# Kernel optimization log

Hardware: AMD Instinct MI355X
Metric: run time of the kernel (lower is better)

The kernel has to match this reference:

```python
import jax, jax.numpy as jnp
import numpy as np

HIDDEN = 1024
NUM_HEADS = 16
HEAD_DIM = HIDDEN // NUM_HEADS
ROPE_BASE = 10000.0
LN_EPS = 1e-8


def _rope_cos_sin(seq_len, dim, dtype=jnp.float32):
    inv_freq = 1.0 / (ROPE_BASE ** (jnp.arange(0, dim, 2, dtype=jnp.float32) / dim))
    t = jnp.arange(seq_len, dtype=jnp.float32)
    freqs = jnp.einsum('i,j->ij', t, inv_freq)          # [S, dim/2]
    emb = jnp.concatenate([freqs, freqs], axis=-1)       # [S, dim]
    return jnp.cos(emb).astype(dtype), jnp.sin(emb).astype(dtype)


def _rotate_half(x):
    x1, x2 = jnp.split(x, 2, axis=-1)
    return jnp.concatenate([-x2, x1], axis=-1)


def setup_inputs() -> dict:
    key = jax.random.key(0)
    ks = jax.random.split(key, 8)
    B, S, H = 4, 2048, HIDDEN
    x = jax.random.normal(ks[0], (B, S, H), dtype=jnp.float32)
    # causal mask, True = attend
    attn_mask = jnp.tril(jnp.ones((S, S), dtype=bool))[None].repeat(B, axis=0)
    lim_p = 1.0 / np.sqrt(H)
    Wp = jax.random.uniform(ks[1], (H, 4 * H), minval=-lim_p, maxval=lim_p, dtype=jnp.float32)
    bp = jax.random.uniform(ks[2], (4 * H,), minval=-lim_p, maxval=lim_p, dtype=jnp.float32)
    ln_g = jnp.ones((H,), dtype=jnp.float32)
    ln_b = jnp.zeros((H,), dtype=jnp.float32)
    Wt = jax.random.uniform(ks[3], (H, H), minval=-lim_p, maxval=lim_p, dtype=jnp.float32)
    bt = jax.random.uniform(ks[4], (H,), minval=-lim_p, maxval=lim_p, dtype=jnp.float32)
    return {"x": x, "attn_mask": attn_mask, "Wp": Wp, "bp": bp,
            "ln_g": ln_g, "ln_b": ln_b, "Wt": Wt, "bt": bt}


def reference(x, attn_mask, Wp, bp, ln_g, ln_b, Wt, bt):
    B, S, H = x.shape
    nh, hd = NUM_HEADS, HEAD_DIM
    proj = x @ Wp + bp                                   # [B,S,4H]
    U, V, Q, K = jnp.split(proj, 4, axis=-1)
    # [B, nh, S, hd]
    Q = Q.reshape(B, S, nh, hd).transpose(0, 2, 1, 3)
    K = K.reshape(B, S, nh, hd).transpose(0, 2, 1, 3)
    V = V.reshape(B, S, nh, hd).transpose(0, 2, 1, 3)
    cos, sin = _rope_cos_sin(S, hd, x.dtype)             # [S, hd]
    Qr = Q * cos + _rotate_half(Q) * sin
    Kr = K * cos + _rotate_half(K) * sin
    scale = hd ** -0.5
    scores = jnp.einsum('bhqd,bhkd->bhqk', Qr, Kr) * scale
    # masked positions -> sigmoid(-inf) == 0; use where for grad safety
    attn = jnp.where(attn_mask[:, None, :, :], jax.nn.sigmoid(scores), 0.0)
    attn_out = jnp.einsum('bhqk,bhkd->bhqd', attn, V)
    attn_out = attn_out.transpose(0, 2, 1, 3).reshape(B, S, H)
    mu = jnp.mean(attn_out, axis=-1, keepdims=True)
    var = jnp.var(attn_out, axis=-1, keepdims=True)
    attn_out = (attn_out - mu) / jnp.sqrt(var + LN_EPS) * ln_g + ln_b
    gated = jax.nn.silu(U) * attn_out
    out = gated @ Wt + bt
    return x + out
```

## Files before the change

### kernel.cpp

```cpp
#include <hip/hip_runtime.h>
#include <math.h>

#define H 1024
#define NH 16
#define HD 64
#define B_ 4
#define S_ 2048
#define ROWS (B_*S_)

#define QSCALE (-0.1803368801111664f)
#define ROPE_C (9.210340371976184f / 32.0f)

typedef __bf16 bf16x2_t __attribute__((ext_vector_type(2)));
typedef __bf16 bf16x4_t __attribute__((ext_vector_type(4)));
typedef __bf16 bf16x8_t __attribute__((ext_vector_type(8)));
typedef float floatx4_t __attribute__((ext_vector_type(4)));

#define GLOAD_LDS16(gp, lp)                                                        \
    __builtin_amdgcn_global_load_lds(                                              \
        (const __attribute__((address_space(1))) unsigned int*)(gp),               \
        (__attribute__((address_space(3))) unsigned int*)(lp), 16, 0, 0)

__global__ __launch_bounds__(256)
void convert_x(const float* __restrict__ src, __bf16* __restrict__ dst)
{
    int i = blockIdx.x * blockDim.x + threadIdx.x;
    float4 v = *reinterpret_cast<const float4*>(&src[(size_t)i * 4]);
    bf16x4_t w = { (__bf16)v.x, (__bf16)v.y, (__bf16)v.z, (__bf16)v.w };
    *reinterpret_cast<bf16x4_t*>(&dst[(size_t)i * 4]) = w;
}

__global__ __launch_bounds__(256)
void transpose_cvt(const float* __restrict__ W, __bf16* __restrict__ Wt, int K, int N)
{
    __shared__ __bf16 t[32][33];
    const int tx = threadIdx.x & 31, ty = threadIdx.x >> 5;
    const int bn = blockIdx.x * 32, bk = blockIdx.y * 32;
#pragma unroll
    for (int i = 0; i < 4; i++) {
        int r = ty + i * 8;
        t[tx][r] = (__bf16)W[(size_t)(bk + r) * N + bn + tx];
    }
    __syncthreads();
#pragma unroll
    for (int i = 0; i < 4; i++) {
        int r = ty + i * 8;
        Wt[(size_t)(bn + r) * K + bk + tx] = t[r][tx];
    }
}


__global__ __launch_bounds__(256)
void gemm_out(const __bf16* __restrict__ A, const __bf16* __restrict__ Bt,
              const float* __restrict__ bias, const float* __restrict__ resid,
              float* __restrict__ C, int M, int N, int K)
{
    __shared__ __bf16 As[128 * 32];
    __shared__ __bf16 Bs[128 * 32];

    const int tid  = threadIdx.x;
    const int wave = tid >> 6, lane = tid & 63;
    const int quad = lane >> 4, ln = lane & 15;
    const int wm = wave & 1, wn = wave >> 1;
    const int m0 = blockIdx.y * 128, n0 = blockIdx.x * 128;

    const int srow = lane >> 2;
    const int skc  = (((lane & 3) ^ ((srow >> 1) & 3)) * 8);
    const int qsw  = (quad ^ ((ln >> 1) & 3)) * 8;

    floatx4_t acc[4][4];
#pragma unroll
    for (int i = 0; i < 4; i++)
#pragma unroll
        for (int j = 0; j < 4; j++) acc[i][j] = (floatx4_t){0.f, 0.f, 0.f, 0.f};

    for (int k0 = 0; k0 < K; k0 += 32) {
#pragma unroll
        for (int p = 0; p < 2; p++) {
            int i = wave * 2 + p;
            int rl = i * 16 + srow;
            GLOAD_LDS16(A  + (size_t)(m0 + rl) * K + k0 + skc, &As[i * 512]);
            GLOAD_LDS16(Bt + (size_t)(n0 + rl) * K + k0 + skc, &Bs[i * 512]);
        }
        __syncthreads();

        bf16x8_t af[4], bf[4];
#pragma unroll
        for (int mt = 0; mt < 4; mt++)
            af[mt] = *reinterpret_cast<const bf16x8_t*>(&As[(wm * 64 + mt * 16 + ln) * 32 + qsw]);
#pragma unroll
        for (int nt = 0; nt < 4; nt++)
            bf[nt] = *reinterpret_cast<const bf16x8_t*>(&Bs[(wn * 64 + nt * 16 + ln) * 32 + qsw]);
#pragma unroll
        for (int mt = 0; mt < 4; mt++)
#pragma unroll
            for (int nt = 0; nt < 4; nt++)
                acc[mt][nt] = __builtin_amdgcn_mfma_f32_16x16x32_bf16(af[mt], bf[nt], acc[mt][nt], 0, 0, 0);
        __syncthreads();
    }

#pragma unroll
    for (int mt = 0; mt < 4; mt++) {
#pragma unroll
        for (int nt = 0; nt < 4; nt++) {
            int col = n0 + wn * 64 + nt * 16 + ln;
            float bv = bias[col];
#pragma unroll
            for (int reg = 0; reg < 4; reg++) {
                int row = m0 + wm * 64 + mt * 16 + quad * 4 + reg;
                float v = acc[mt][nt][reg] + bv + resid[(size_t)row * N + col];
                C[(size_t)row * N + col] = v;
            }
        }
    }
}

__global__ __launch_bounds__(256)
void gemm_proj(const __bf16* __restrict__ A, const __bf16* __restrict__ Bt,
               const float* __restrict__ bias,
               __bf16* __restrict__ Ug, __bf16* __restrict__ Vh,
               __bf16* __restrict__ Qh, __bf16* __restrict__ Kh)
{
    const int M = ROWS, N = 4096, K = 1024;
    __shared__ __bf16 As[128 * 32];
    __shared__ __bf16 Bs[128 * 32];

    const int tid  = threadIdx.x;
    const int wave = tid >> 6, lane = tid & 63;
    const int quad = lane >> 4, ln = lane & 15;
    const int wm = wave & 1, wn = wave >> 1;
    const int m0 = blockIdx.y * 128, n0 = blockIdx.x * 128;

    const int srow = lane >> 2;
    const int skc  = (((lane & 3) ^ ((srow >> 1) & 3)) * 8);
    const int qsw  = (quad ^ ((ln >> 1) & 3)) * 8;

    floatx4_t acc[4][4];
#pragma unroll
    for (int i = 0; i < 4; i++)
#pragma unroll
        for (int j = 0; j < 4; j++) acc[i][j] = (floatx4_t){0.f, 0.f, 0.f, 0.f};

    for (int k0 = 0; k0 < K; k0 += 32) {
#pragma unroll
        for (int p = 0; p < 2; p++) {
            int i = wave * 2 + p;
            int rl = i * 16 + srow;
            GLOAD_LDS16(A  + (size_t)(m0 + rl) * K + k0 + skc, &As[i * 512]);
            GLOAD_LDS16(Bt + (size_t)(n0 + rl) * K + k0 + skc, &Bs[i * 512]);
        }
        __syncthreads();

        bf16x8_t af[4], bf[4];
#pragma unroll
        for (int mt = 0; mt < 4; mt++)
            af[mt] = *reinterpret_cast<const bf16x8_t*>(&As[(wm * 64 + mt * 16 + ln) * 32 + qsw]);
#pragma unroll
        for (int nt = 0; nt < 4; nt++)
            bf[nt] = *reinterpret_cast<const bf16x8_t*>(&Bs[(wn * 64 + nt * 16 + ln) * 32 + qsw]);
#pragma unroll
        for (int mt = 0; mt < 4; mt++)
#pragma unroll
            for (int nt = 0; nt < 4; nt++)
                acc[mt][nt] = __builtin_amdgcn_mfma_f32_16x16x32_bf16(af[mt], bf[nt], acc[mt][nt], 0, 0, 0);
        __syncthreads();
    }

    float bv[4];
#pragma unroll
    for (int nt = 0; nt < 4; nt++) bv[nt] = bias[n0 + wn * 64 + nt * 16 + ln];

    if (n0 < 1024) {
#pragma unroll
        for (int mt = 0; mt < 4; mt++)
#pragma unroll
            for (int nt = 0; nt < 4; nt++) {
                int col = n0 + wn * 64 + nt * 16 + ln;
#pragma unroll
                for (int reg = 0; reg < 4; reg++) {
                    int row = m0 + wm * 64 + mt * 16 + quad * 4 + reg;
                    Ug[(size_t)row * 1024 + col] = (__bf16)(acc[mt][nt][reg] + bv[nt]);
                }
            }
    } else if (n0 < 2048) {
        const int h = ((n0 - 1024) >> 6) + wn;
#pragma unroll
        for (int mt = 0; mt < 4; mt++)
#pragma unroll
            for (int reg = 0; reg < 4; reg++) {
                int row = m0 + wm * 64 + mt * 16 + quad * 4 + reg;
                int b = row >> 11, s = row & (S_ - 1);
                size_t orow = ((size_t)(b * NH + h) * S_ + s) * 64;
#pragma unroll
                for (int nt = 0; nt < 4; nt++)
                    Vh[orow + nt * 16 + ln] = (__bf16)(acc[mt][nt][reg] + bv[nt]);
            }
    } else {
        const bool isQ = (n0 < 3072);
        const int h = ((n0 - (isQ ? 2048 : 3072)) >> 6) + wn;
        __bf16* dst = isQ ? Qh : Kh;
        const float sc = isQ ? QSCALE : 1.0f;
        const float inv0 = __expf(-(float)ln * ROPE_C);
        const float inv1 = __expf(-(float)(16 + ln) * ROPE_C);
#pragma unroll
        for (int mt = 0; mt < 4; mt++)
#pragma unroll
            for (int reg = 0; reg < 4; reg++) {
                int row = m0 + wm * 64 + mt * 16 + quad * 4 + reg;
                int b = row >> 11, s = row & (S_ - 1);
                size_t orow = ((size_t)(b * NH + h) * S_ + s) * 64;
                float sn0, cs0, sn1, cs1;
                __sincosf((float)s * inv0, &sn0, &cs0);
                __sincosf((float)s * inv1, &sn1, &cs1);
                float lo0 = acc[0][0][reg], hi0 = acc[0][2][reg];
                float lo1 = acc[0][1][reg], hi1 = acc[0][3][reg];
                lo0 = acc[mt][0][reg] + bv[0]; hi0 = acc[mt][2][reg] + bv[2];
                lo1 = acc[mt][1][reg] + bv[1]; hi1 = acc[mt][3][reg] + bv[3];
                dst[orow + ln]      = (__bf16)((lo0 * cs0 - hi0 * sn0) * sc);
                dst[orow + 32 + ln] = (__bf16)((hi0 * cs0 + lo0 * sn0) * sc);
                dst[orow + 16 + ln] = (__bf16)((lo1 * cs1 - hi1 * sn1) * sc);
                dst[orow + 48 + ln] = (__bf16)((hi1 * cs1 + lo1 * sn1) * sc);
            }
    }
}

__global__ __launch_bounds__(256)
void transpose_v(const __bf16* __restrict__ Vh, __bf16* __restrict__ VtG)
{
    const int tid = threadIdx.x;
    const int st = blockIdx.x, bh = blockIdx.y;
    const int s0 = st * 64;
    const int d = tid & 63, k16 = tid >> 6;
    __bf16 vals[16];
#pragma unroll
    for (int j = 0; j < 16; j++) {
        int k = s0 + k16 * 16 + j;
        vals[j] = Vh[((size_t)bh * S_ + k) * 64 + d];
    }
    size_t orow = ((size_t)(bh * 64 + d)) * S_ + s0 + k16 * 16;
    *reinterpret_cast<bf16x8_t*>(&VtG[orow])     = *reinterpret_cast<bf16x8_t*>(&vals[0]);
    *reinterpret_cast<bf16x8_t*>(&VtG[orow + 8]) = *reinterpret_cast<bf16x8_t*>(&vals[8]);
}

__global__ __launch_bounds__(256)
void attn_mfma(const __bf16* __restrict__ Qh, const __bf16* __restrict__ Kh,
               const __bf16* __restrict__ VtG, __bf16* __restrict__ attn_out)
{
    __shared__ __bf16 Ks[4096];
    __shared__ __bf16 Vt[4096];
    __shared__ __bf16 Ps[4][32][72];

    const int tid = threadIdx.x, wave = tid >> 6, lane = tid & 63;
    const int quad = lane >> 4, ln = lane & 15;
    const int qt = (S_ / 128 - 1) - (blockIdx.x >> 6);
    const int hb = blockIdx.x & 63, h = hb & 15, b = hb >> 4, bh = b * NH + h;
    const int Q0 = qt * 128, T0 = 2 * qt;
    const int wl = wave * 16 + ln;

    const size_t qr = ((size_t)bh * S_ + Q0 + wl) * 64;
    bf16x8_t qa[2][2];
    qa[0][0] = *reinterpret_cast<const bf16x8_t*>(&Qh[qr + quad * 8]);
    qa[0][1] = *reinterpret_cast<const bf16x8_t*>(&Qh[qr + 32 + quad * 8]);
    qa[1][0] = *reinterpret_cast<const bf16x8_t*>(&Qh[qr + 4096 + quad * 8]);
    qa[1][1] = *reinterpret_cast<const bf16x8_t*>(&Qh[qr + 4096 + 32 + quad * 8]);

    const int sr = lane >> 3, scl = (lane & 7) ^ sr;
    const int c0 = wave * 2, c1 = c0 + 1;
    const size_t khead = (size_t)bh * S_ * 64;
    const int koff0 = (c0 * 8 + sr) * 64 + scl * 8;
    const int koff1 = (c1 * 8 + sr) * 64 + scl * 8;
    const size_t vg0 = ((size_t)bh * 64 + c0 * 8 + sr) * S_ + scl * 8;
    const size_t vg1 = ((size_t)bh * 64 + c1 * 8 + sr) * S_ + scl * 8;

    const int m7 = ln & 7;
    int ka[4][2];
#pragma unroll
    for (int nt = 0; nt < 4; nt++) {
        int row = nt * 16 + ln;
        ka[nt][0] = row * 64 + ((quad ^ m7) << 3);
        ka[nt][1] = row * 64 + (((quad + 4) ^ m7) << 3);
    }

    floatx4_t o[2][4];
#pragma unroll
    for (int s = 0; s < 2; s++)
#pragma unroll
        for (int dt = 0; dt < 4; dt++) o[s][dt] = (floatx4_t){0.f, 0.f, 0.f, 0.f};

    for (int kt = 0; kt <= T0 + 1; kt++) {
        __syncthreads();
        const size_t kg = khead + (size_t)kt * 4096;
        GLOAD_LDS16(Kh  + kg + koff0, &Ks[c0 * 512]);
        GLOAD_LDS16(Kh  + kg + koff1, &Ks[c1 * 512]);
        GLOAD_LDS16(VtG + vg0 + kt * 64, &Vt[c0 * 512]);
        GLOAD_LDS16(VtG + vg1 + kt * 64, &Vt[c1 * 512]);
        __syncthreads();

        bf16x8_t kf[4][2];
#pragma unroll
        for (int nt = 0; nt < 4; nt++) {
            kf[nt][0] = *reinterpret_cast<const bf16x8_t*>(&Ks[ka[nt][0]]);
            kf[nt][1] = *reinterpret_cast<const bf16x8_t*>(&Ks[ka[nt][1]]);
        }
        bf16x8_t vf[4][2];
#pragma unroll
        for (int dt = 0; dt < 4; dt++) {
            vf[dt][0] = *reinterpret_cast<const bf16x8_t*>(&Vt[ka[dt][0]]);
            vf[dt][1] = *reinterpret_cast<const bf16x8_t*>(&Vt[ka[dt][1]]);
        }

        const int mode0 = (kt < T0) ? 0 : ((kt == T0) ? 1 : 2);
        const int mode1 = (kt <= T0) ? 0 : 1;

#pragma unroll
        for (int s = 0; s < 2; s++) {
            const int mode = s ? mode1 : mode0;
            if (mode == 2) continue;

            floatx4_t st[4];
#pragma unroll
            for (int nt = 0; nt < 4; nt++) {
                floatx4_t acc = (floatx4_t){0.f, 0.f, 0.f, 0.f};
                acc = __builtin_amdgcn_mfma_f32_16x16x32_bf16(kf[nt][0], qa[s][0], acc, 0, 0, 0);
                acc = __builtin_amdgcn_mfma_f32_16x16x32_bf16(kf[nt][1], qa[s][1], acc, 0, 0, 0);
                st[nt] = acc;
            }

#pragma unroll
            for (int nt = 0; nt < 4; nt++) {
                bf16x4_t pk;
#pragma unroll
                for (int r = 0; r < 4; r++) {
                    float a = st[nt][r];
                    if (mode == 1) {
                        int kl = nt * 16 + quad * 4 + r;
                        a = (kl <= wl) ? a : __builtin_inff();
                    }
                    float p = __builtin_amdgcn_rcpf(1.f + __builtin_amdgcn_exp2f(a));
                    pk[r] = (__bf16)p;
                }
                *reinterpret_cast<bf16x4_t*>(&Ps[wave][s * 16 + ln][nt * 16 + quad * 4]) = pk;
            }

            const __bf16* prow = &Ps[wave][s * 16 + ln][quad * 8];
            bf16x8_t p0 = *reinterpret_cast<const bf16x8_t*>(prow);
            bf16x8_t p1 = *reinterpret_cast<const bf16x8_t*>(prow + 32);
#pragma unroll
            for (int dt = 0; dt < 4; dt++) {
                o[s][dt] = __builtin_amdgcn_mfma_f32_16x16x32_bf16(p0, vf[dt][0], o[s][dt], 0, 0, 0);
                o[s][dt] = __builtin_amdgcn_mfma_f32_16x16x32_bf16(p1, vf[dt][1], o[s][dt], 0, 0, 0);
            }
        }
    }

#pragma unroll
    for (int s = 0; s < 2; s++) {
        const int qrow_g = b * S_ + Q0 + s * 64 + wave * 16 + quad * 4;
#pragma unroll
        for (int dt = 0; dt < 4; dt++) {
#pragma unroll
            for (int reg = 0; reg < 4; reg++) {
                attn_out[(size_t)(qrow_g + reg) * H + h * 64 + dt * 16 + ln] =
                    (__bf16)o[s][dt][reg];
            }
        }
    }
}

__global__ __launch_bounds__(256)
void ln_gate_kernel(const __bf16* __restrict__ attn_out, const __bf16* __restrict__ Ug,
                    const float* __restrict__ ln_g, const float* __restrict__ ln_b,
                    __bf16* __restrict__ gated)
{
    const int row = blockIdx.x;
    const int tid = threadIdx.x;

    bf16x4_t vb = *reinterpret_cast<const bf16x4_t*>(&attn_out[(size_t)row * H + tid * 4]);
    float v0 = (float)vb[0], v1 = (float)vb[1], v2 = (float)vb[2], v3 = (float)vb[3];
    float s  = v0 + v1 + v2 + v3;
    float sq = v0 * v0 + v1 * v1 + v2 * v2 + v3 * v3;
#pragma unroll
    for (int off = 32; off > 0; off >>= 1) {
        s  += __shfl_down(s, off);
        sq += __shfl_down(sq, off);
    }
    __shared__ float ps[4], pq[4];
    int wave = tid >> 6, lane = tid & 63;
    if (lane == 0) { ps[wave] = s; pq[wave] = sq; }
    __syncthreads();
    float ts = ps[0] + ps[1] + ps[2] + ps[3];
    float tq = pq[0] + pq[1] + pq[2] + pq[3];
    float mu  = ts * (1.f / (float)H);
    float var = tq * (1.f / (float)H) - mu * mu;
    float rstd = rsqrtf(var + 1e-8f);

    bf16x4_t ub = *reinterpret_cast<const bf16x4_t*>(&Ug[(size_t)row * 1024 + tid * 4]);
    float4 g  = *reinterpret_cast<const float4*>(&ln_g[tid * 4]);
    float4 bb = *reinterpret_cast<const float4*>(&ln_b[tid * 4]);
    float u0 = (float)ub[0], u1 = (float)ub[1], u2 = (float)ub[2], u3 = (float)ub[3];
    bf16x4_t outv;
    outv[0] = (__bf16)(((v0 - mu) * rstd * g.x + bb.x) * (u0 / (1.f + __expf(-u0))));
    outv[1] = (__bf16)(((v1 - mu) * rstd * g.y + bb.y) * (u1 / (1.f + __expf(-u1))));
    outv[2] = (__bf16)(((v2 - mu) * rstd * g.z + bb.z) * (u2 / (1.f + __expf(-u2))));
    outv[3] = (__bf16)(((v3 - mu) * rstd * g.w + bb.w) * (u3 / (1.f + __expf(-u3))));
    *reinterpret_cast<bf16x4_t*>(&gated[(size_t)row * H + tid * 4]) = outv;
}

extern "C" void kernel_launch(void* const* d_in, const int* in_sizes, int n_in,
                              void* d_out, int out_size, void* d_ws, size_t ws_size,
                              hipStream_t stream)
{
    const float* x    = (const float*)d_in[0];
    const float* Wp   = (const float*)d_in[2];
    const float* bp   = (const float*)d_in[3];
    const float* ln_g = (const float*)d_in[4];
    const float* ln_b = (const float*)d_in[5];
    const float* Wt   = (const float*)d_in[6];
    const float* bt   = (const float*)d_in[7];
    float* out = (float*)d_out;

    char* ws = (char*)d_ws;
    const size_t MB = 1024 * 1024;
    __bf16* Ug    = (__bf16*)(ws);
    __bf16* Vh    = (__bf16*)(ws + 16  * MB);
    __bf16* Qh    = (__bf16*)(ws + 32  * MB);
    __bf16* Kh    = (__bf16*)(ws + 48  * MB);
    __bf16* attn  = (__bf16*)(ws + 64  * MB);
    __bf16* gated = (__bf16*)(ws + 80  * MB);
    __bf16* VtG   = (__bf16*)(ws + 96  * MB);
    __bf16* Ax    = (__bf16*)(ws + 112 * MB);
    __bf16* Wp_t  = (__bf16*)(ws + 128 * MB);
    __bf16* Wt_t  = (__bf16*)(ws + 136 * MB);

    convert_x<<<(ROWS * H / 4) / 256, 256, 0, stream>>>(x, Ax);
    transpose_cvt<<<dim3(4096 / 32, 1024 / 32), 256, 0, stream>>>(Wp, Wp_t, 1024, 4096);
    transpose_cvt<<<dim3(1024 / 32, 1024 / 32), 256, 0, stream>>>(Wt, Wt_t, 1024, 1024);

    dim3 g1(4096 / 128, ROWS / 128);
    gemm_proj<<<g1, 256, 0, stream>>>(Ax, Wp_t, bp, Ug, Vh, Qh, Kh);

    transpose_v<<<dim3(S_ / 64, B_ * NH), 256, 0, stream>>>(Vh, VtG);

    attn_mfma<<<(S_ / 128) * NH * B_, 256, 0, stream>>>(Qh, Kh, VtG, attn);

    ln_gate_kernel<<<ROWS, 256, 0, stream>>>(attn, Ug, ln_g, ln_b, gated);

    dim3 g3(1024 / 128, ROWS / 128);
    gemm_out<<<g3, 256, 0, stream>>>(gated, Wt_t, bt, x, out, ROWS, 1024, 1024);
}
```

Before: 345.2 us.

## Double-buffer LDS tiles in GEMMs and attention, merge prep kernels into one launch

Both GEMM kernels and the attention kernel now use two LDS buffers. The next K tile is fetched with global_load_lds while MFMAs run on the current tile, which removes one barrier per iteration. The three preprocessing kernels (x conversion and two weight transposes) are merged into one launch dispatched by block index, and the per-wave P scratch in attention is shrunk to 16 rows. This doubles LDS use per block, which may reduce occupancy, in exchange for overlapping memory latency with compute.

Measured after the change: 343.7 us. Within noise of the previous version (-0.4%).

```diff
diff --git a/kernel.cpp b/kernel.cpp
--- a/kernel.cpp
+++ b/kernel.cpp
@@ -22,20 +22,31 @@
         (__attribute__((address_space(3))) unsigned int*)(lp), 16, 0, 0)
 
 __global__ __launch_bounds__(256)
-void convert_x(const float* __restrict__ src, __bf16* __restrict__ dst)
-{
-    int i = blockIdx.x * blockDim.x + threadIdx.x;
-    float4 v = *reinterpret_cast<const float4*>(&src[(size_t)i * 4]);
-    bf16x4_t w = { (__bf16)v.x, (__bf16)v.y, (__bf16)v.z, (__bf16)v.w };
-    *reinterpret_cast<bf16x4_t*>(&dst[(size_t)i * 4]) = w;
-}
-
-__global__ __launch_bounds__(256)
-void transpose_cvt(const float* __restrict__ W, __bf16* __restrict__ Wt, int K, int N)
+void prep_kernel(const float* __restrict__ x, const float* __restrict__ Wp,
+                 const float* __restrict__ Wt,
+                 __bf16* __restrict__ Ax, __bf16* __restrict__ Wp_t,
+                 __bf16* __restrict__ Wt_t)
 {
     __shared__ __bf16 t[32][33];
-    const int tx = threadIdx.x & 31, ty = threadIdx.x >> 5;
-    const int bn = blockIdx.x * 32, bk = blockIdx.y * 32;
+    const int flat = blockIdx.x;
+    const int tid = threadIdx.x;
+
+    if (flat < 8192) {
+        size_t i = (size_t)flat * 256 + tid;
+        float4 v = *reinterpret_cast<const float4*>(&x[i * 4]);
+        bf16x4_t w = { (__bf16)v.x, (__bf16)v.y, (__bf16)v.z, (__bf16)v.w };
+        *reinterpret_cast<bf16x4_t*>(&Ax[i * 4]) = w;
+        return;
+    }
+    const float* W; __bf16* Wo; int K, N, bn, bk;
+    if (flat < 12288) {
+        int id = flat - 8192;  W = Wp; Wo = Wp_t; K = 1024; N = 4096;
+        bn = (id & 127) * 32;  bk = (id >> 7) * 32;
+    } else {
+        int id = flat - 12288; W = Wt; Wo = Wt_t; K = 1024; N = 1024;
+        bn = (id & 31) * 32;   bk = (id >> 5) * 32;
+    }
+    const int tx = tid & 31, ty = tid >> 5;
 #pragma unroll
     for (int i = 0; i < 4; i++) {
         int r = ty + i * 8;
@@ -45,7 +56,7 @@
 #pragma unroll
     for (int i = 0; i < 4; i++) {
         int r = ty + i * 8;
-        Wt[(size_t)(bn + r) * K + bk + tx] = t[r][tx];
+        Wo[(size_t)(bn + r) * K + bk + tx] = t[r][tx];
     }
 }
 
@@ -55,8 +66,8 @@
               const float* __restrict__ bias, const float* __restrict__ resid,
               float* __restrict__ C, int M, int N, int K)
 {
-    __shared__ __bf16 As[128 * 32];
-    __shared__ __bf16 Bs[128 * 32];
+    __shared__ __bf16 As[2][4096];
+    __shared__ __bf16 Bs[2][4096];
 
     const int tid  = threadIdx.x;
     const int wave = tid >> 6, lane = tid & 63;
@@ -68,35 +79,45 @@
     const int skc  = (((lane & 3) ^ ((srow >> 1) & 3)) * 8);
     const int qsw  = (quad ^ ((ln >> 1) & 3)) * 8;
 
+    const int i0 = wave * 2, i1 = i0 + 1;
+    const size_t ga0 = (size_t)(m0 + i0 * 16 + srow) * K + skc;
+    const size_t ga1 = (size_t)(m0 + i1 * 16 + srow) * K + skc;
+    const size_t gb0 = (size_t)(n0 + i0 * 16 + srow) * K + skc;
+    const size_t gb1 = (size_t)(n0 + i1 * 16 + srow) * K + skc;
+
     floatx4_t acc[4][4];
 #pragma unroll
     for (int i = 0; i < 4; i++)
 #pragma unroll
         for (int j = 0; j < 4; j++) acc[i][j] = (floatx4_t){0.f, 0.f, 0.f, 0.f};
 
-    for (int k0 = 0; k0 < K; k0 += 32) {
-#pragma unroll
-        for (int p = 0; p < 2; p++) {
-            int i = wave * 2 + p;
-            int rl = i * 16 + srow;
-            GLOAD_LDS16(A  + (size_t)(m0 + rl) * K + k0 + skc, &As[i * 512]);
-            GLOAD_LDS16(Bt + (size_t)(n0 + rl) * K + k0 + skc, &Bs[i * 512]);
-        }
+    GLOAD_LDS16(A  + ga0, &As[0][i0 * 512]);
+    GLOAD_LDS16(A  + ga1, &As[0][i1 * 512]);
+    GLOAD_LDS16(Bt + gb0, &Bs[0][i0 * 512]);
+    GLOAD_LDS16(Bt + gb1, &Bs[0][i1 * 512]);
+
+    int buf = 0;
+    for (int k0 = 0; k0 < K; k0 += 32, buf ^= 1) {
         __syncthreads();
-
+        if (k0 + 32 < K) {
+            int nb = buf ^ 1, kn = k0 + 32;
+            GLOAD_LDS16(A  + ga0 + kn, &As[nb][i0 * 512]);
+            GLOAD_LDS16(A  + ga1 + kn, &As[nb][i1 * 512]);
+            GLOAD_LDS16(Bt + gb0 + kn, &Bs[nb][i0 * 512]);
+            GLOAD_LDS16(Bt + gb1 + kn, &Bs[nb][i1 * 512]);
+        }
         bf16x8_t af[4], bf[4];
 #pragma unroll
         for (int mt = 0; mt < 4; mt++)
-            af[mt] = *reinterpret_cast<const bf16x8_t*>(&As[(wm * 64 + mt * 16 + ln) * 32 + qsw]);
+            af[mt] = *reinterpret_cast<const bf16x8_t*>(&As[buf][(wm * 64 + mt * 16 + ln) * 32 + qsw]);
 #pragma unroll
         for (int nt = 0; nt < 4; nt++)
-            bf[nt] = *reinterpret_cast<const bf16x8_t*>(&Bs[(wn * 64 + nt * 16 + ln) * 32 + qsw]);
+            bf[nt] = *reinterpret_cast<const bf16x8_t*>(&Bs[buf][(wn * 64 + nt * 16 + ln) * 32 + qsw]);
 #pragma unroll
         for (int mt = 0; mt < 4; mt++)
 #pragma unroll
             for (int nt = 0; nt < 4; nt++)
                 acc[mt][nt] = __builtin_amdgcn_mfma_f32_16x16x32_bf16(af[mt], bf[nt], acc[mt][nt], 0, 0, 0);
-        __syncthreads();
     }
 
 #pragma unroll
@@ -108,8 +129,7 @@
 #pragma unroll
             for (int reg = 0; reg < 4; reg++) {
                 int row = m0 + wm * 64 + mt * 16 + quad * 4 + reg;
-                float v = acc[mt][nt][reg] + bv + resid[(size_t)row * N + col];
-                C[(size_t)row * N + col] = v;
+                C[(size_t)row * N + col] = acc[mt][nt][reg] + bv + resid[(size_t)row * N + col];
             }
         }
     }
@@ -121,9 +141,9 @@
                __bf16* __restrict__ Ug, __bf16* __restrict__ Vh,
                __bf16* __restrict__ Qh, __bf16* __restrict__ Kh)
 {
-    const int M = ROWS, N = 4096, K = 1024;
-    __shared__ __bf16 As[128 * 32];
-    __shared__ __bf16 Bs[128 * 32];
+    const int K = 1024;
+    __shared__ __bf16 As[2][4096];
+    __shared__ __bf16 Bs[2][4096];
 
     const int tid  = threadIdx.x;
     const int wave = tid >> 6, lane = tid & 63;
@@ -135,35 +155,45 @@
     const int skc  = (((lane & 3) ^ ((srow >> 1) & 3)) * 8);
     const int qsw  = (quad ^ ((ln >> 1) & 3)) * 8;
 
+    const int i0 = wave * 2, i1 = i0 + 1;
+    const size_t ga0 = (size_t)(m0 + i0 * 16 + srow) * K + skc;
+    const size_t ga1 = (size_t)(m0 + i1 * 16 + srow) * K + skc;
+    const size_t gb0 = (size_t)(n0 + i0 * 16 + srow) * K + skc;
+    const size_t gb1 = (size_t)(n0 + i1 * 16 + srow) * K + skc;
+
     floatx4_t acc[4][4];
 #pragma unroll
     for (int i = 0; i < 4; i++)
 #pragma unroll
         for (int j = 0; j < 4; j++) acc[i][j] = (floatx4_t){0.f, 0.f, 0.f, 0.f};
 
-    for (int k0 = 0; k0 < K; k0 += 32) {
-#pragma unroll
-        for (int p = 0; p < 2; p++) {
-            int i = wave * 2 + p;
-            int rl = i * 16 + srow;
-            GLOAD_LDS16(A  + (size_t)(m0 + rl) * K + k0 + skc, &As[i * 512]);
-            GLOAD_LDS16(Bt + (size_t)(n0 + rl) * K + k0 + skc, &Bs[i * 512]);
-        }
+    GLOAD_LDS16(A  + ga0, &As[0][i0 * 512]);
+    GLOAD_LDS16(A  + ga1, &As[0][i1 * 512]);
+    GLOAD_LDS16(Bt + gb0, &Bs[0][i0 * 512]);
+    GLOAD_LDS16(Bt + gb1, &Bs[0][i1 * 512]);
+
+    int buf = 0;
+    for (int k0 = 0; k0 < K; k0 += 32, buf ^= 1) {
         __syncthreads();
-
+        if (k0 + 32 < K) {
+            int nb = buf ^ 1, kn = k0 + 32;
+            GLOAD_LDS16(A  + ga0 + kn, &As[nb][i0 * 512]);
+            GLOAD_LDS16(A  + ga1 + kn, &As[nb][i1 * 512]);
+            GLOAD_LDS16(Bt + gb0 + kn, &Bs[nb][i0 * 512]);
+            GLOAD_LDS16(Bt + gb1 + kn, &Bs[nb][i1 * 512]);
+        }
         bf16x8_t af[4], bf[4];
 #pragma unroll
         for (int mt = 0; mt < 4; mt++)
-            af[mt] = *reinterpret_cast<const bf16x8_t*>(&As[(wm * 64 + mt * 16 + ln) * 32 + qsw]);
+            af[mt] = *reinterpret_cast<const bf16x8_t*>(&As[buf][(wm * 64 + mt * 16 + ln) * 32 + qsw]);
 #pragma unroll
         for (int nt = 0; nt < 4; nt++)
-            bf[nt] = *reinterpret_cast<const bf16x8_t*>(&Bs[(wn * 64 + nt * 16 + ln) * 32 + qsw]);
+            bf[nt] = *reinterpret_cast<const bf16x8_t*>(&Bs[buf][(wn * 64 + nt * 16 + ln) * 32 + qsw]);
 #pragma unroll
         for (int mt = 0; mt < 4; mt++)
 #pragma unroll
             for (int nt = 0; nt < 4; nt++)
                 acc[mt][nt] = __builtin_amdgcn_mfma_f32_16x16x32_bf16(af[mt], bf[nt], acc[mt][nt], 0, 0, 0);
-        __syncthreads();
     }
 
     float bv[4];
@@ -212,10 +242,8 @@
                 float sn0, cs0, sn1, cs1;
                 __sincosf((float)s * inv0, &sn0, &cs0);
                 __sincosf((float)s * inv1, &sn1, &cs1);
-                float lo0 = acc[0][0][reg], hi0 = acc[0][2][reg];
-                float lo1 = acc[0][1][reg], hi1 = acc[0][3][reg];
-                lo0 = acc[mt][0][reg] + bv[0]; hi0 = acc[mt][2][reg] + bv[2];
-                lo1 = acc[mt][1][reg] + bv[1]; hi1 = acc[mt][3][reg] + bv[3];
+                float lo0 = acc[mt][0][reg] + bv[0], hi0 = acc[mt][2][reg] + bv[2];
+                float lo1 = acc[mt][1][reg] + bv[1], hi1 = acc[mt][3][reg] + bv[3];
                 dst[orow + ln]      = (__bf16)((lo0 * cs0 - hi0 * sn0) * sc);
                 dst[orow + 32 + ln] = (__bf16)((hi0 * cs0 + lo0 * sn0) * sc);
                 dst[orow + 16 + ln] = (__bf16)((lo1 * cs1 - hi1 * sn1) * sc);
@@ -246,9 +274,9 @@
 void attn_mfma(const __bf16* __restrict__ Qh, const __bf16* __restrict__ Kh,
                const __bf16* __restrict__ VtG, __bf16* __restrict__ attn_out)
 {
-    __shared__ __bf16 Ks[4096];
-    __shared__ __bf16 Vt[4096];
-    __shared__ __bf16 Ps[4][32][72];
+    __shared__ __bf16 Ks[2][4096];
+    __shared__ __bf16 Vt[2][4096];
+    __shared__ __bf16 Ps[4][16][72];
 
     const int tid = threadIdx.x, wave = tid >> 6, lane = tid & 63;
     const int quad = lane >> 4, ln = lane & 15;
@@ -287,26 +315,33 @@
 #pragma unroll
         for (int dt = 0; dt < 4; dt++) o[s][dt] = (floatx4_t){0.f, 0.f, 0.f, 0.f};
 
+    GLOAD_LDS16(Kh  + khead + koff0, &Ks[0][c0 * 512]);
+    GLOAD_LDS16(Kh  + khead + koff1, &Ks[0][c1 * 512]);
+    GLOAD_LDS16(VtG + vg0,           &Vt[0][c0 * 512]);
+    GLOAD_LDS16(VtG + vg1,           &Vt[0][c1 * 512]);
+
     for (int kt = 0; kt <= T0 + 1; kt++) {
+        const int buf = kt & 1;
         __syncthreads();
-        const size_t kg = khead + (size_t)kt * 4096;
-        GLOAD_LDS16(Kh  + kg + koff0, &Ks[c0 * 512]);
-        GLOAD_LDS16(Kh  + kg + koff1, &Ks[c1 * 512]);
-        GLOAD_LDS16(VtG + vg0 + kt * 64, &Vt[c0 * 512]);
-        GLOAD_LDS16(VtG + vg1 + kt * 64, &Vt[c1 * 512]);
-        __syncthreads();
-
-        bf16x8_t kf[4][2];
+        if (kt <= T0) {
+            const int nb = buf ^ 1;
+            const size_t kg = khead + (size_t)(kt + 1) * 4096;
+            GLOAD_LDS16(Kh  + kg + koff0,            &Ks[nb][c0 * 512]);
+            GLOAD_LDS16(Kh  + kg + koff1,            &Ks[nb][c1 * 512]);
+            GLOAD_LDS16(VtG + vg0 + (kt + 1) * 64,   &Vt[nb][c0 * 512]);
+            GLOAD_LDS16(VtG + vg1 + (kt + 1) * 64,   &Vt[nb][c1 * 512]);
+        }
+
+        bf16x8_t kf[4][2], vf[4][2];
 #pragma unroll
         for (int nt = 0; nt < 4; nt++) {
-            kf[nt][0] = *reinterpret_cast<const bf16x8_t*>(&Ks[ka[nt][0]]);
-            kf[nt][1] = *reinterpret_cast<const bf16x8_t*>(&Ks[ka[nt][1]]);
-        }
-        bf16x8_t vf[4][2];
+            kf[nt][0] = *reinterpret_cast<const bf16x8_t*>(&Ks[buf][ka[nt][0]]);
+            kf[nt][1] = *reinterpret_cast<const bf16x8_t*>(&Ks[buf][ka[nt][1]]);
+        }
 #pragma unroll
         for (int dt = 0; dt < 4; dt++) {
-            vf[dt][0] = *reinterpret_cast<const bf16x8_t*>(&Vt[ka[dt][0]]);
-            vf[dt][1] = *reinterpret_cast<const bf16x8_t*>(&Vt[ka[dt][1]]);
+            vf[dt][0] = *reinterpret_cast<const bf16x8_t*>(&Vt[buf][ka[dt][0]]);
+            vf[dt][1] = *reinterpret_cast<const bf16x8_t*>(&Vt[buf][ka[dt][1]]);
         }
 
         const int mode0 = (kt < T0) ? 0 : ((kt == T0) ? 1 : 2);
@@ -339,10 +374,10 @@
                     float p = __builtin_amdgcn_rcpf(1.f + __builtin_amdgcn_exp2f(a));
                     pk[r] = (__bf16)p;
                 }
-                *reinterpret_cast<bf16x4_t*>(&Ps[wave][s * 16 + ln][nt * 16 + quad * 4]) = pk;
-            }
-
-            const __bf16* prow = &Ps[wave][s * 16 + ln][quad * 8];
+                *reinterpret_cast<bf16x4_t*>(&Ps[wave][ln][nt * 16 + quad * 4]) = pk;
+            }
+
+            const __bf16* prow = &Ps[wave][ln][quad * 8];
             bf16x8_t p0 = *reinterpret_cast<const bf16x8_t*>(prow);
             bf16x8_t p1 = *reinterpret_cast<const bf16x8_t*>(prow + 32);
 #pragma unroll
@@ -432,9 +467,7 @@
     __bf16* Wp_t  = (__bf16*)(ws + 128 * MB);
     __bf16* Wt_t  = (__bf16*)(ws + 136 * MB);
 
-    convert_x<<<(ROWS * H / 4) / 256, 256, 0, stream>>>(x, Ax);
-    transpose_cvt<<<dim3(4096 / 32, 1024 / 32), 256, 0, stream>>>(Wp, Wp_t, 1024, 4096);
-    transpose_cvt<<<dim3(1024 / 32, 1024 / 32), 256, 0, stream>>>(Wt, Wt_t, 1024, 1024);
+    prep_kernel<<<13312, 256, 0, stream>>>(x, Wp, Wt, Ax, Wp_t, Wt_t);
 
     dim3 g1(4096 / 128, ROWS / 128);
     gemm_proj<<<g1, 256, 0, stream>>>(Ax, Wp_t, bp, Ug, Vh, Qh, Kh);
```
